# Performance work log

Hardware: AMD Instinct MI355X
Metric: run time of the kernel (lower is better)

## Reference

```python
import jax, jax.numpy as jnp
import numpy as np

DIM = 256
HEADS = 4
DIM_HEADS = 32
HIDDEN = HEADS * DIM_HEADS


def setup_inputs() -> dict:
    key = jax.random.key(0)
    k0, k1, k2, k3, k4, k5, k6 = jax.random.split(key, 7)
    b, c, h, w = 16, DIM, 64, 64
    s = 1.0 / np.sqrt(DIM)
    return {
        "x": jax.random.normal(k0, (b, c, h, w), dtype=jnp.float32),
        "Wq": jax.random.normal(k1, (HIDDEN, DIM), dtype=jnp.float32) * s,
        "Wk": jax.random.normal(k2, (HIDDEN, DIM), dtype=jnp.float32) * s,
        "Wv": jax.random.normal(k3, (HIDDEN, DIM), dtype=jnp.float32) * s,
        "Wo": jax.random.normal(k4, (DIM, HIDDEN), dtype=jnp.float32) / np.sqrt(HIDDEN),
        "bo": jax.random.normal(k5, (DIM,), dtype=jnp.float32) * 0.01,
        "g": jnp.ones((DIM,), dtype=jnp.float32),
    }


def reference(x, Wq, Wk, Wv, Wo, bo, g):
    b, c, h, w = x.shape
    n = h * w
    scale = DIM_HEADS ** (-0.5)
    xf = x.reshape(b, c, n)  # [b,c,n]
    # 1x1 convs == channel matmuls
    q = jnp.einsum('dc,bcn->bdn', Wq, xf).reshape(b, HEADS, DIM_HEADS, n)
    k = jnp.einsum('dc,bcn->bdn', Wk, xf).reshape(b, HEADS, DIM_HEADS, n)
    v = jnp.einsum('dc,bcn->bdn', Wv, xf).reshape(b, HEADS, DIM_HEADS, n)
    q = jax.nn.softmax(q, axis=-2) * scale  # softmax over head-dim
    k = jax.nn.softmax(k, axis=-1)          # softmax over tokens
    v = v / n
    context = jnp.einsum('bhdn,bhen->bhde', k, v)  # [b,h,dh,dh]
    out = jnp.einsum('bhde,bhdn->bhen', context, q)  # [b,h,dh,n]
    out = out.reshape(b, HIDDEN, n)
    out = jnp.einsum('cd,bdn->bcn', Wo, out) + bo[None, :, None]
    # LayerNorm over channel dim (biased var, eps=1e-5 for fp32)
    eps = 1e-5
    mean = jnp.mean(out, axis=1, keepdims=True)
    var = jnp.var(out, axis=1, keepdims=True)
    out = (out - mean) * jax.lax.rsqrt(var + eps) * g[None, :, None]
    return out.reshape(b, c, h, w)
```

## Files before the change

### kernel.cpp

```cpp
#include <hip/hip_runtime.h>
#include <hip/hip_bf16.h>

typedef float f32x4 __attribute__((ext_vector_type(4)));
typedef short bf16x8 __attribute__((ext_vector_type(8)));
typedef unsigned short us4 __attribute__((ext_vector_type(4)));

#define NB 16
#define NC 256
#define NTOK 4096
#define NHID 128

__device__ __forceinline__ unsigned pk2(float lo, float hi) {
  float2 f; f.x = lo; f.y = hi;
  __hip_bfloat162 h = __float22bfloat162_rn(f);
  unsigned u; __builtin_memcpy(&u, &h, 4); return u;
}
__device__ __forceinline__ uint2 pk4(f32x4 v) {
  uint2 r; r.x = pk2(v[0], v[1]); r.y = pk2(v[2], v[3]); return r;
}
__device__ __forceinline__ float bf2f(unsigned short h) {
  union { unsigned u; float f; } v; v.u = ((unsigned)h) << 16;
  return v.f;
}

__global__ __launch_bounds__(512) void k0_w(
    const float* __restrict__ Wq, const float* __restrict__ Wk,
    const float* __restrict__ Wv, unsigned short* __restrict__ Wswz)
{
  const int mt = blockIdx.x;
  const int t = threadIdx.x;
  const int ks = t >> 6, l = t & 63;
  const int m = mt * 16 + (l & 15);
  const int col = ks * 32 + (l >> 4) * 8;
  const float* src = (m < 128) ? (Wq + (size_t)m * NC)
                   : (m < 256) ? (Wk + (size_t)(m - 128) * NC)
                               : (Wv + (size_t)(m - 256) * NC);
  const float4 w0 = *(const float4*)(src + col);
  const float4 w1 = *(const float4*)(src + col + 4);
  uint4 p;
  p.x = pk2(w0.x, w0.y); p.y = pk2(w0.z, w0.w);
  p.z = pk2(w1.x, w1.y); p.w = pk2(w1.z, w1.w);
  *(uint4*)&Wswz[((size_t)(mt * 8 + ks)) * 512 + l * 8] = p;
}

__global__ __launch_bounds__(512, 4) void k1_qkv(
    const float* __restrict__ x, const unsigned short* __restrict__ Wswz,
    unsigned short* __restrict__ qg, unsigned short* __restrict__ Pp,
    float* __restrict__ Sp)
{
  __shared__ __align__(16) unsigned char smem[65536];

  const int tile = blockIdx.x, b = blockIdx.y;
  const int n0 = tile * 64;
  const int t = threadIdx.x;
  const int wid = t >> 6, l = t & 63;
  const int l16 = l & 15, lhi = l >> 4;
  const unsigned xr = (unsigned)((l16 & 7) << 4);

  int fr[3];
  if (wid < 4) { fr[0] = 2 * wid; fr[1] = 2 * wid + 1; fr[2] = 8 + wid; }
  else { const int w = wid - 4; fr[0] = 12 + w; fr[1] = 16 + 2 * w; fr[2] = 17 + 2 * w; }

#define WFRAG(f, kss) (*(const bf16x8*)&Wswz[((size_t)(fr[f] * 8 + (kss))) * 512 + l * 8])
#define AFRAG(tf, kss) (*(const bf16x8*)(smem + \
    (((unsigned)(((tf) * 16 + l16) * 512 + (kss) * 64 + lhi * 16)) ^ xr)))
#define PKVB(roww, boff) (smem + 32768u + \
    ((((unsigned)((roww) * 128 + (boff))) ^ (((unsigned)((roww) & 7)) << 4))))

  {
    const int cg = t >> 4;
    const int tq = t & 15;
    const float* rp = x + (size_t)b * NC * NTOK + (size_t)(cg * 8) * NTOK + n0 + tq * 4;
    float4 rv[8];
#pragma unroll
    for (int i = 0; i < 8; ++i) rv[i] = *(const float4*)(rp + (size_t)i * NTOK);
#pragma unroll
    for (int j = 0; j < 4; ++j) {
      const int tok = tq * 4 + j;
      uint4 pv;
      pv.x = pk2(rv[0][j], rv[1][j]); pv.y = pk2(rv[2][j], rv[3][j]);
      pv.z = pk2(rv[4][j], rv[5][j]); pv.w = pk2(rv[6][j], rv[7][j]);
      *(uint4*)(smem + (((unsigned)(tok * 512 + cg * 16)) ^ ((unsigned)(tok & 7) << 4))) = pv;
    }
  }
  __syncthreads();

  f32x4 acc[4][3];
#pragma unroll
  for (int i = 0; i < 4; ++i)
#pragma unroll
    for (int j = 0; j < 3; ++j) acc[i][j] = 0;

  bf16x8 w0[3], w1[3];
#pragma unroll
  for (int f = 0; f < 3; ++f) w0[f] = WFRAG(f, 0);

#pragma unroll
  for (int kk = 0; kk < 4; ++kk) {
    const int ke = 2 * kk, ko = 2 * kk + 1;
#pragma unroll
    for (int f = 0; f < 3; ++f) w1[f] = WFRAG(f, ko);
#pragma unroll
    for (int tf = 0; tf < 4; ++tf) {
      const bf16x8 a = AFRAG(tf, ke);
#pragma unroll
      for (int f = 0; f < 3; ++f)
        acc[tf][f] = __builtin_amdgcn_mfma_f32_16x16x32_bf16(a, w0[f], acc[tf][f], 0, 0, 0);
    }
    if (kk < 3) {
#pragma unroll
      for (int f = 0; f < 3; ++f) w0[f] = WFRAG(f, ke + 2);
    }
#pragma unroll
    for (int tf = 0; tf < 4; ++tf) {
      const bf16x8 a = AFRAG(tf, ko);
#pragma unroll
      for (int f = 0; f < 3; ++f)
        acc[tf][f] = __builtin_amdgcn_mfma_f32_16x16x32_bf16(a, w1[f], acc[tf][f], 0, 0, 0);
    }
  }

  const float qscale = 0.1767766952966369f;
  if (wid < 4) {
#pragma unroll
    for (int tf = 0; tf < 4; ++tf)
#pragma unroll
      for (int r = 0; r < 4; ++r) {
        const float a0 = acc[tf][0][r], a1 = acc[tf][1][r];
        float mx = fmaxf(a0, a1);
        mx = fmaxf(mx, __shfl_xor(mx, 1));
        mx = fmaxf(mx, __shfl_xor(mx, 2));
        mx = fmaxf(mx, __shfl_xor(mx, 4));
        mx = fmaxf(mx, __shfl_xor(mx, 8));
        const float e0 = __expf(a0 - mx), e1 = __expf(a1 - mx);
        float s = e0 + e1;
        s += __shfl_xor(s, 1); s += __shfl_xor(s, 2);
        s += __shfl_xor(s, 4); s += __shfl_xor(s, 8);
        const float inv = qscale / s;
        acc[tf][0][r] = e0 * inv;
        acc[tf][1][r] = e1 * inv;
      }
    float s = 0.f;
#pragma unroll
    for (int tf = 0; tf < 4; ++tf)
#pragma unroll
      for (int r = 0; r < 4; ++r) {
        const float e = __expf(acc[tf][2][r]);
        acc[tf][2][r] = e;
        s += e;
      }
    s += __shfl_xor(s, 16);
    s += __shfl_xor(s, 32);
    if (l < 16) Sp[((size_t)b * 64 + tile) * 128 + (fr[2] - 8) * 16 + l16] = s;

    unsigned short* qt = qg + ((size_t)(b * 64 + tile)) * 8192;
#pragma unroll
    for (int f = 0; f < 2; ++f) {
      const int j = fr[f] * 16 + l16;
#pragma unroll
      for (int tf = 0; tf < 4; ++tf)
        *(uint2*)&qt[tf * 2048 + j * 16 + lhi * 4] = pk4(acc[tf][f]);
    }
    const int row = (fr[2] - 8) * 16 + l16;
#pragma unroll
    for (int tf = 0; tf < 4; ++tf)
      *(uint2*)PKVB(row, tf * 32 + lhi * 8) = pk4(acc[tf][2]);
  } else {
    float s = 0.f;
#pragma unroll
    for (int tf = 0; tf < 4; ++tf)
#pragma unroll
      for (int r = 0; r < 4; ++r) {
        const float e = __expf(acc[tf][0][r]);
        acc[tf][0][r] = e;
        s += e;
      }
    s += __shfl_xor(s, 16);
    s += __shfl_xor(s, 32);
    if (l < 16) Sp[((size_t)b * 64 + tile) * 128 + (fr[0] - 8) * 16 + l16] = s;

    const int rowk = (fr[0] - 8) * 16 + l16;
    const int rowv1 = 128 + (fr[1] - 16) * 16 + l16;
    const int rowv2 = 128 + (fr[2] - 16) * 16 + l16;
#pragma unroll
    for (int tf = 0; tf < 4; ++tf) {
      *(uint2*)PKVB(rowk, tf * 32 + lhi * 8) = pk4(acc[tf][0]);
      *(uint2*)PKVB(rowv1, tf * 32 + lhi * 8) = pk4(acc[tf][1]);
      *(uint2*)PKVB(rowv2, tf * 32 + lhi * 8) = pk4(acc[tf][2]);
    }
  }
  __syncthreads();

  {
    const int h = wid & 3, dh = wid >> 2;
    f32x4 ca[2];
    ca[0] = 0; ca[1] = 0;
#pragma unroll
    for (int ks2 = 0; ks2 < 2; ++ks2) {
      const int rowa = h * 32 + dh * 16 + l16;
      const bf16x8 ae = *(const bf16x8*)PKVB(rowa, ks2 * 64 + lhi * 16);
#pragma unroll
      for (int e = 0; e < 2; ++e) {
        const int rowb = 128 + h * 32 + e * 16 + l16;
        const bf16x8 be = *(const bf16x8*)PKVB(rowb, ks2 * 64 + lhi * 16);
        ca[e] = __builtin_amdgcn_mfma_f32_16x16x32_bf16(ae, be, ca[e], 0, 0, 0);
      }
    }
    unsigned short* pb = Pp + (((size_t)b * 64 + tile) * 4 + h) * 1024;
#pragma unroll
    for (int e = 0; e < 2; ++e)
      *(uint2*)&pb[(e * 16 + l16) * 32 + dh * 16 + lhi * 4] = pk4(ca[e]);
  }
}

__global__ __launch_bounds__(256) void k2a_tree(
    const unsigned short* __restrict__ Pp, const float* __restrict__ Sp,
    float* __restrict__ Pr, float* __restrict__ Sr)
{
  const int seg = blockIdx.x, b = blockIdx.y;
  const int t = threadIdx.x;
  const unsigned short* pb = Pp + ((size_t)b * 64 + seg * 8) * 4096;
  f32x4 a[4];
#pragma unroll
  for (int i = 0; i < 4; ++i) a[i] = 0;
#pragma unroll
  for (int tile = 0; tile < 8; ++tile) {
#pragma unroll
    for (int i = 0; i < 4; ++i) {
      const us4 v = *(const us4*)&pb[tile * 4096 + i * 1024 + t * 4];
      a[i][0] += bf2f(v[0]); a[i][1] += bf2f(v[1]);
      a[i][2] += bf2f(v[2]); a[i][3] += bf2f(v[3]);
    }
  }
  float* pr = Pr + ((size_t)b * 8 + seg) * 4096;
#pragma unroll
  for (int i = 0; i < 4; ++i) *(f32x4*)&pr[i * 1024 + t * 4] = a[i];

  if (t < 128) {
    float s = 0.f;
    const float* sb = Sp + ((size_t)b * 64 + seg * 8) * 128 + t;
#pragma unroll
    for (int i = 0; i < 8; ++i) s += sb[i * 128];
    Sr[((size_t)b * 8 + seg) * 128 + t] = s;
  }
}

__global__ __launch_bounds__(256) void k2bc(
    const float* __restrict__ Pr, const float* __restrict__ Sr,
    const float* __restrict__ Wo, unsigned short* __restrict__ Mswz)
{
  __shared__ float CnS[4096];
  __shared__ float Ss[128];
  const int ct = blockIdx.x, b = blockIdx.y;
  const int t = threadIdx.x;

  if (t < 128) {
    float s = 0.f;
    const float* sb = Sr + (size_t)b * 8 * 128 + t;
#pragma unroll
    for (int i = 0; i < 8; ++i) s += sb[i * 128];
    Ss[t] = 1.0f / (s * 4096.0f);
  }
  __syncthreads();

#pragma unroll
  for (int i = 0; i < 16; ++i) {
    const int idx = t + 256 * i;
    float a = 0.f;
#pragma unroll
    for (int seg = 0; seg < 8; ++seg) a += Pr[((size_t)b * 8 + seg) * 4096 + idx];
    CnS[idx] = a * Ss[((idx >> 10) << 5) | (idx & 31)];
  }
  __syncthreads();

  const int ks = t >> 6, l = t & 63;
  const int c = ct * 16 + (l & 15);
  const int d0 = (l >> 4) * 8;
  const float* wr = Wo + (size_t)c * NHID + ks * 32;
  const float* cb = &CnS[ks * 1024];
  f32x4 s0 = 0, s1 = 0;
#pragma unroll 8
  for (int e = 0; e < 32; ++e) {
    const float w = wr[e];
    const f32x4 c0 = *(const f32x4*)&cb[e * 32 + d0];
    const f32x4 c1 = *(const f32x4*)&cb[e * 32 + d0 + 4];
#pragma unroll
    for (int j = 0; j < 4; ++j) { s0[j] += w * c0[j]; s1[j] += w * c1[j]; }
  }
  uint4 p;
  p.x = pk2(s0[0], s0[1]); p.y = pk2(s0[2], s0[3]);
  p.z = pk2(s1[0], s1[1]); p.w = pk2(s1[2], s1[3]);
  *(uint4*)&Mswz[(((size_t)b * 16 + ct) * 4 + ks) * 512 + l * 8] = p;
}

__global__ __launch_bounds__(256, 3) void k3_out(
    const unsigned short* __restrict__ qg, const unsigned short* __restrict__ Mswz,
    const float* __restrict__ bo, const float* __restrict__ g, float* __restrict__ out)
{
  __shared__ __align__(16) unsigned char qs[16384];
  __shared__ float red[4 * 64 * 2];
  const int bx = blockIdx.x, b = blockIdx.y;
  const int t = threadIdx.x;
  const int wid = t >> 6, l = t & 63;
  const int l16 = l & 15, lhi = l >> 4;

  bf16x8 mf[4][4];
#pragma unroll
  for (int cf = 0; cf < 4; ++cf)
#pragma unroll
    for (int ks = 0; ks < 4; ++ks)
      mf[cf][ks] = *(const bf16x8*)&Mswz[(((size_t)b * 16 + wid * 4 + cf) * 4 + ks) * 512 + l * 8];

  float bol[4], gl[4];
#pragma unroll
  for (int cf = 0; cf < 4; ++cf) {
    const int c = wid * 64 + cf * 16 + l16;
    bol[cf] = bo[c]; gl[cf] = g[c];
  }

  for (int tl = 0; tl < 2; ++tl) {
    const int tile = bx * 2 + tl;

    {
      const unsigned char* gq = (const unsigned char*)(qg + ((size_t)(b * 64 + tile)) * 8192);
#pragma unroll
      for (int i = 0; i < 4; ++i)
        *(uint4*)(qs + t * 16 + i * 4096) = *(const uint4*)(gq + t * 16 + i * 4096);
    }

    f32x4 acc[4][4];
#pragma unroll
    for (int i = 0; i < 4; ++i)
#pragma unroll
      for (int j = 0; j < 4; ++j) acc[i][j] = 0;

    __syncthreads();

#pragma unroll
    for (int tf = 0; tf < 4; ++tf) {
      bf16x8 qf[4];
#pragma unroll
      for (int ks = 0; ks < 4; ++ks) {
        bf16x8 qv;
#pragma unroll
        for (int jj = 0; jj < 8; ++jj) {
          const unsigned short u = *(const unsigned short*)(qs +
              tf * 4096 + (ks * 32 + lhi * 8 + jj) * 32 + l16 * 2);
          qv[jj] = (short)u;
        }
        qf[ks] = qv;
      }
#pragma unroll
      for (int ks = 0; ks < 4; ++ks)
#pragma unroll
        for (int cf = 0; cf < 4; ++cf)
          acc[tf][cf] = __builtin_amdgcn_mfma_f32_16x16x32_bf16(qf[ks], mf[cf][ks], acc[tf][cf], 0, 0, 0);
    }

#pragma unroll
    for (int tf = 0; tf < 4; ++tf)
#pragma unroll
      for (int cf = 0; cf < 4; ++cf)
#pragma unroll
        for (int r = 0; r < 4; ++r) acc[tf][cf][r] += bol[cf];

    __syncthreads();

#pragma unroll
    for (int tf = 0; tf < 4; ++tf)
#pragma unroll
      for (int r = 0; r < 4; ++r) {
        float s = 0.f, q2 = 0.f;
#pragma unroll
        for (int cf = 0; cf < 4; ++cf) {
          const float v = acc[tf][cf][r];
          s += v; q2 += v * v;
        }
        s += __shfl_xor(s, 1); q2 += __shfl_xor(q2, 1);
        s += __shfl_xor(s, 2); q2 += __shfl_xor(q2, 2);
        s += __shfl_xor(s, 4); q2 += __shfl_xor(q2, 4);
        s += __shfl_xor(s, 8); q2 += __shfl_xor(q2, 8);
        if (l16 == 0) {
          const int tok = tf * 16 + lhi * 4 + r;
          red[(wid * 64 + tok) * 2] = s;
          red[(wid * 64 + tok) * 2 + 1] = q2;
        }
      }
    __syncthreads();

    float mean[4][4], rstd[4][4];
#pragma unroll
    for (int tf = 0; tf < 4; ++tf)
#pragma unroll
      for (int r = 0; r < 4; ++r) {
        const int tok = tf * 16 + lhi * 4 + r;
        float s = 0.f, q2 = 0.f;
#pragma unroll
        for (int cg = 0; cg < 4; ++cg) {
          s += red[(cg * 64 + tok) * 2];
          q2 += red[(cg * 64 + tok) * 2 + 1];
        }
        const float mu = s * (1.0f / 256.0f);
        const float var = q2 * (1.0f / 256.0f) - mu * mu;
        mean[tf][r] = mu;
        rstd[tf][r] = rsqrtf(var + 1e-5f);
      }

    float* ob = out + ((size_t)b * NC) * NTOK + tile * 64;
#pragma unroll
    for (int tf = 0; tf < 4; ++tf)
#pragma unroll
      for (int cf = 0; cf < 4; ++cf) {
        const int c = wid * 64 + cf * 16 + l16;
        f32x4 ov;
#pragma unroll
        for (int r = 0; r < 4; ++r)
          ov[r] = (acc[tf][cf][r] - mean[tf][r]) * rstd[tf][r] * gl[cf];
        *(f32x4*)&ob[(size_t)c * NTOK + tf * 16 + lhi * 4] = ov;
      }
    __syncthreads();
  }
}

extern "C" void kernel_launch(void* const* d_in, const int* in_sizes, int n_in,
                              void* d_out, int out_size, void* d_ws, size_t ws_size,
                              hipStream_t stream) {
  const float* x  = (const float*)d_in[0];
  const float* Wq = (const float*)d_in[1];
  const float* Wk = (const float*)d_in[2];
  const float* Wv = (const float*)d_in[3];
  const float* Wo = (const float*)d_in[4];
  const float* bo = (const float*)d_in[5];
  const float* g  = (const float*)d_in[6];
  float* out = (float*)d_out;

  char* ws = (char*)d_ws;
  unsigned short* Wswz = (unsigned short*)(ws);
  unsigned short* qg   = (unsigned short*)(ws + 262144);
  unsigned short* Pp   = (unsigned short*)(ws + 17039360);
  float*          Sp   = (float*)(ws + 25427968);
  float*          Pr   = (float*)(ws + 25952256);
  float*          Sr   = (float*)(ws + 28049408);
  unsigned short* Mswz = (unsigned short*)(ws + 28377088);
  (void)ws_size; (void)in_sizes; (void)n_in; (void)out_size;

  hipLaunchKernelGGL(k0_w, dim3(24), dim3(512), 0, stream, Wq, Wk, Wv, Wswz);
  hipLaunchKernelGGL(k1_qkv, dim3(64, NB), dim3(512), 0, stream, x, Wswz, qg, Pp, Sp);
  hipLaunchKernelGGL(k2a_tree, dim3(8, NB), dim3(256), 0, stream, Pp, Sp, Pr, Sr);
  hipLaunchKernelGGL(k2bc, dim3(16, NB), dim3(256), 0, stream, Pr, Sr, Wo, Mswz);
  hipLaunchKernelGGL(k3_out, dim3(32, NB), dim3(256), 0, stream, qg, Mswz, bo, g, out);
}
```

Baseline: 86.51 us.

## Give each k3_out block one tile and deepen the W-fragment prefetch in k1

The output kernel now handles one 64-token tile per block instead of two, and the grid doubles to 64x16. The q-tile load is issued before the Mswz fragment loads so the two overlap. This raises parallelism and removes the per-tile loop with its trailing barrier, but each block now reloads the M fragments for only one tile. In k1_qkv the weight-fragment pipeline becomes a three-stage rotating prefetch running two k-steps ahead, at the cost of more registers.

```diff
diff --git a/kernel.cpp b/kernel.cpp
--- a/kernel.cpp
+++ b/kernel.cpp
@@ -91,33 +91,27 @@
 #pragma unroll
     for (int j = 0; j < 3; ++j) acc[i][j] = 0;
 
-  bf16x8 w0[3], w1[3];
-#pragma unroll
-  for (int f = 0; f < 3; ++f) w0[f] = WFRAG(f, 0);
-
-#pragma unroll
-  for (int kk = 0; kk < 4; ++kk) {
-    const int ke = 2 * kk, ko = 2 * kk + 1;
-#pragma unroll
-    for (int f = 0; f < 3; ++f) w1[f] = WFRAG(f, ko);
+  bf16x8 wA[3], wB[3], wC[3];
+#pragma unroll
+  for (int f = 0; f < 3; ++f) wA[f] = WFRAG(f, 0);
+#pragma unroll
+  for (int f = 0; f < 3; ++f) wB[f] = WFRAG(f, 1);
+
+#pragma unroll
+  for (int ks = 0; ks < 8; ++ks) {
+    if (ks < 6) {
+#pragma unroll
+      for (int f = 0; f < 3; ++f) wC[f] = WFRAG(f, ks + 2);
+    }
 #pragma unroll
     for (int tf = 0; tf < 4; ++tf) {
-      const bf16x8 a = AFRAG(tf, ke);
+      const bf16x8 a = AFRAG(tf, ks);
 #pragma unroll
       for (int f = 0; f < 3; ++f)
-        acc[tf][f] = __builtin_amdgcn_mfma_f32_16x16x32_bf16(a, w0[f], acc[tf][f], 0, 0, 0);
-    }
-    if (kk < 3) {
-#pragma unroll
-      for (int f = 0; f < 3; ++f) w0[f] = WFRAG(f, ke + 2);
-    }
-#pragma unroll
-    for (int tf = 0; tf < 4; ++tf) {
-      const bf16x8 a = AFRAG(tf, ko);
-#pragma unroll
-      for (int f = 0; f < 3; ++f)
-        acc[tf][f] = __builtin_amdgcn_mfma_f32_16x16x32_bf16(a, w1[f], acc[tf][f], 0, 0, 0);
-    }
+        acc[tf][f] = __builtin_amdgcn_mfma_f32_16x16x32_bf16(a, wA[f], acc[tf][f], 0, 0, 0);
+    }
+#pragma unroll
+    for (int f = 0; f < 3; ++f) { wA[f] = wB[f]; wB[f] = wC[f]; }
   }
 
   const float qscale = 0.1767766952966369f;
@@ -304,12 +298,48 @@
   const int wid = t >> 6, l = t & 63;
   const int l16 = l & 15, lhi = l >> 4;
 
+  {
+    const unsigned char* gq = (const unsigned char*)(qg + ((size_t)(b * 64 + bx)) * 8192);
+#pragma unroll
+    for (int i = 0; i < 4; ++i)
+      *(uint4*)(qs + t * 16 + i * 4096) = *(const uint4*)(gq + t * 16 + i * 4096);
+  }
+
   bf16x8 mf[4][4];
 #pragma unroll
   for (int cf = 0; cf < 4; ++cf)
 #pragma unroll
     for (int ks = 0; ks < 4; ++ks)
       mf[cf][ks] = *(const bf16x8*)&Mswz[(((size_t)b * 16 + wid * 4 + cf) * 4 + ks) * 512 + l * 8];
+
+  f32x4 acc[4][4];
+#pragma unroll
+  for (int i = 0; i < 4; ++i)
+#pragma unroll
+    for (int j = 0; j < 4; ++j) acc[i][j] = 0;
+
+  __syncthreads();
+
+#pragma unroll
+  for (int tf = 0; tf < 4; ++tf) {
+    bf16x8 qf[4];
+#pragma unroll
+    for (int ks = 0; ks < 4; ++ks) {
+      bf16x8 qv;
+#pragma unroll
+      for (int jj = 0; jj < 8; ++jj) {
+        const unsigned short u = *(const unsigned short*)(qs +
+            tf * 4096 + (ks * 32 + lhi * 8 + jj) * 32 + l16 * 2);
+        qv[jj] = (short)u;
+      }
+      qf[ks] = qv;
+    }
+#pragma unroll
+    for (int ks = 0; ks < 4; ++ks)
+#pragma unroll
+      for (int cf = 0; cf < 4; ++cf)
+        acc[tf][cf] = __builtin_amdgcn_mfma_f32_16x16x32_bf16(qf[ks], mf[cf][ks], acc[tf][cf], 0, 0, 0);
+  }
 
   float bol[4], gl[4];
 #pragma unroll
@@ -317,109 +347,67 @@
     const int c = wid * 64 + cf * 16 + l16;
     bol[cf] = bo[c]; gl[cf] = g[c];
   }
-
-  for (int tl = 0; tl < 2; ++tl) {
-    const int tile = bx * 2 + tl;
-
-    {
-      const unsigned char* gq = (const unsigned char*)(qg + ((size_t)(b * 64 + tile)) * 8192);
-#pragma unroll
-      for (int i = 0; i < 4; ++i)
-        *(uint4*)(qs + t * 16 + i * 4096) = *(const uint4*)(gq + t * 16 + i * 4096);
-    }
-
-    f32x4 acc[4][4];
-#pragma unroll
-    for (int i = 0; i < 4; ++i)
-#pragma unroll
-      for (int j = 0; j < 4; ++j) acc[i][j] = 0;
-
-    __syncthreads();
-
-#pragma unroll
-    for (int tf = 0; tf < 4; ++tf) {
-      bf16x8 qf[4];
-#pragma unroll
-      for (int ks = 0; ks < 4; ++ks) {
-        bf16x8 qv;
-#pragma unroll
-        for (int jj = 0; jj < 8; ++jj) {
-          const unsigned short u = *(const unsigned short*)(qs +
-              tf * 4096 + (ks * 32 + lhi * 8 + jj) * 32 + l16 * 2);
-          qv[jj] = (short)u;
-        }
-        qf[ks] = qv;
-      }
-#pragma unroll
-      for (int ks = 0; ks < 4; ++ks)
-#pragma unroll
-        for (int cf = 0; cf < 4; ++cf)
-          acc[tf][cf] = __builtin_amdgcn_mfma_f32_16x16x32_bf16(qf[ks], mf[cf][ks], acc[tf][cf], 0, 0, 0);
-    }
-
-#pragma unroll
-    for (int tf = 0; tf < 4; ++tf)
-#pragma unroll
-      for (int cf = 0; cf < 4; ++cf)
-#pragma unroll
-        for (int r = 0; r < 4; ++r) acc[tf][cf][r] += bol[cf];
-
-    __syncthreads();
-
-#pragma unroll
-    for (int tf = 0; tf < 4; ++tf)
-#pragma unroll
-      for (int r = 0; r < 4; ++r) {
-        float s = 0.f, q2 = 0.f;
-#pragma unroll
-        for (int cf = 0; cf < 4; ++cf) {
-          const float v = acc[tf][cf][r];
-          s += v; q2 += v * v;
-        }
-        s += __shfl_xor(s, 1); q2 += __shfl_xor(q2, 1);
-        s += __shfl_xor(s, 2); q2 += __shfl_xor(q2, 2);
-        s += __shfl_xor(s, 4); q2 += __shfl_xor(q2, 4);
-        s += __shfl_xor(s, 8); q2 += __shfl_xor(q2, 8);
-        if (l16 == 0) {
-          const int tok = tf * 16 + lhi * 4 + r;
-          red[(wid * 64 + tok) * 2] = s;
-          red[(wid * 64 + tok) * 2 + 1] = q2;
-        }
-      }
-    __syncthreads();
-
-    float mean[4][4], rstd[4][4];
-#pragma unroll
-    for (int tf = 0; tf < 4; ++tf)
-#pragma unroll
-      for (int r = 0; r < 4; ++r) {
+#pragma unroll
+  for (int tf = 0; tf < 4; ++tf)
+#pragma unroll
+    for (int cf = 0; cf < 4; ++cf)
+#pragma unroll
+      for (int r = 0; r < 4; ++r) acc[tf][cf][r] += bol[cf];
+
+  __syncthreads();
+
+#pragma unroll
+  for (int tf = 0; tf < 4; ++tf)
+#pragma unroll
+    for (int r = 0; r < 4; ++r) {
+      float s = 0.f, q2 = 0.f;
+#pragma unroll
+      for (int cf = 0; cf < 4; ++cf) {
+        const float v = acc[tf][cf][r];
+        s += v; q2 += v * v;
+      }
+      s += __shfl_xor(s, 1); q2 += __shfl_xor(q2, 1);
+      s += __shfl_xor(s, 2); q2 += __shfl_xor(q2, 2);
+      s += __shfl_xor(s, 4); q2 += __shfl_xor(q2, 4);
+      s += __shfl_xor(s, 8); q2 += __shfl_xor(q2, 8);
+      if (l16 == 0) {
         const int tok = tf * 16 + lhi * 4 + r;
-        float s = 0.f, q2 = 0.f;
-#pragma unroll
-        for (int cg = 0; cg < 4; ++cg) {
-          s += red[(cg * 64 + tok) * 2];
-          q2 += red[(cg * 64 + tok) * 2 + 1];
-        }
-        const float mu = s * (1.0f / 256.0f);
-        const float var = q2 * (1.0f / 256.0f) - mu * mu;
-        mean[tf][r] = mu;
-        rstd[tf][r] = rsqrtf(var + 1e-5f);
-      }
-
-    float* ob = out + ((size_t)b * NC) * NTOK + tile * 64;
-#pragma unroll
-    for (int tf = 0; tf < 4; ++tf)
-#pragma unroll
-      for (int cf = 0; cf < 4; ++cf) {
-        const int c = wid * 64 + cf * 16 + l16;
-        f32x4 ov;
-#pragma unroll
-        for (int r = 0; r < 4; ++r)
-          ov[r] = (acc[tf][cf][r] - mean[tf][r]) * rstd[tf][r] * gl[cf];
-        *(f32x4*)&ob[(size_t)c * NTOK + tf * 16 + lhi * 4] = ov;
-      }
-    __syncthreads();
-  }
+        red[(wid * 64 + tok) * 2] = s;
+        red[(wid * 64 + tok) * 2 + 1] = q2;
+      }
+    }
+  __syncthreads();
+
+  float mean[4][4], rstd[4][4];
+#pragma unroll
+  for (int tf = 0; tf < 4; ++tf)
+#pragma unroll
+    for (int r = 0; r < 4; ++r) {
+      const int tok = tf * 16 + lhi * 4 + r;
+      float s = 0.f, q2 = 0.f;
+#pragma unroll
+      for (int cg = 0; cg < 4; ++cg) {
+        s += red[(cg * 64 + tok) * 2];
+        q2 += red[(cg * 64 + tok) * 2 + 1];
+      }
+      const float mu = s * (1.0f / 256.0f);
+      const float var = q2 * (1.0f / 256.0f) - mu * mu;
+      mean[tf][r] = mu;
+      rstd[tf][r] = rsqrtf(var + 1e-5f);
+    }
+
+  float* ob = out + ((size_t)b * NC) * NTOK + bx * 64;
+#pragma unroll
+  for (int tf = 0; tf < 4; ++tf)
+#pragma unroll
+    for (int cf = 0; cf < 4; ++cf) {
+      const int c = wid * 64 + cf * 16 + l16;
+      f32x4 ov;
+#pragma unroll
+      for (int r = 0; r < 4; ++r)
+        ov[r] = (acc[tf][cf][r] - mean[tf][r]) * rstd[tf][r] * gl[cf];
+      *(f32x4*)&ob[(size_t)c * NTOK + tf * 16 + lhi * 4] = ov;
+    }
 }
 
 extern "C" void kernel_launch(void* const* d_in, const int* in_sizes, int n_in,
@@ -448,5 +436,5 @@
   hipLaunchKernelGGL(k1_qkv, dim3(64, NB), dim3(512), 0, stream, x, Wswz, qg, Pp, Sp);
   hipLaunchKernelGGL(k2a_tree, dim3(8, NB), dim3(256), 0, stream, Pp, Sp, Pr, Sr);
   hipLaunchKernelGGL(k2bc, dim3(16, NB), dim3(256), 0, stream, Pr, Sr, Wo, Mswz);
-  hipLaunchKernelGGL(k3_out, dim3(32, NB), dim3(256), 0, stream, qg, Mswz, bo, g, out);
-}
+  hipLaunchKernelGGL(k3_out, dim3(64, NB), dim3(256), 0, stream, qg, Mswz, bo, g, out);
+}
```

Result: faster. 76.58 us (-11.5%).
